# Kernel tuning notes

Hardware: AMD Instinct MI355X
Metric: run time of the kernel (lower is better)

Reference implementation:

```python
import jax, jax.numpy as jnp
import numpy as np

GX = GY = GZ = 128
VOXEL_DIM = 28  # 1 density + 27 SH coefficients (9 per RGB channel)
NUM_RAYS = 8192
NUM_SAMPLES = 128


def sh_basis(theta, phi):
    """Degree-2 SH basis in the coefficient order used by harmonic():
    [Y_0_0, Y_m1_1, Y_0_1, Y_1_1, Y_m2_2, Y_m1_2, Y_0_2, Y_1_2, Y_2_2]."""
    y00 = 0.5 * jnp.sqrt(1.0 / jnp.pi)
    h3 = 0.5 * jnp.sqrt(3.0 / jnp.pi)
    q5 = 0.25 * jnp.sqrt(5.0 / jnp.pi)
    h15 = 0.5 * jnp.sqrt(15.0 / jnp.pi)
    q15 = 0.25 * jnp.sqrt(15.0 / jnp.pi)
    st, ct = jnp.sin(theta), jnp.cos(theta)
    sp, cp = jnp.sin(phi), jnp.cos(phi)
    return jnp.stack([
        y00 * jnp.ones_like(theta),          # Y_0_0
        h3 * st * sp,                        # Y_m1_1
        h3 * ct,                             # Y_0_1
        h3 * st * cp,                        # Y_1_1
        h15 * st * cp * st * sp,             # Y_m2_2
        h15 * st * sp * ct,                  # Y_m1_2
        q5 * (3.0 * ct * ct - 1.0),          # Y_0_2
        h15 * st * cp * ct,                  # Y_1_2
        q15 * ((st * cp) ** 2 - (st * sp) ** 2),  # Y_2_2
    ])


def trilinear(grid, pos):
    """grid: [GX,GY,GZ,D]; pos: [R,S,3] -> [R,S,D] interpolated features."""
    p0 = jnp.floor(pos).astype(jnp.int32)
    fr = pos - p0.astype(pos.dtype)
    x0, y0, z0 = p0[..., 0], p0[..., 1], p0[..., 2]
    xd, yd, zd = fr[..., 0:1], fr[..., 1:2], fr[..., 2:3]
    c000 = grid[x0, y0, z0]
    c001 = grid[x0, y0, z0 + 1]
    c010 = grid[x0, y0 + 1, z0]
    c011 = grid[x0, y0 + 1, z0 + 1]
    c100 = grid[x0 + 1, y0, z0]
    c101 = grid[x0 + 1, y0, z0 + 1]
    c110 = grid[x0 + 1, y0 + 1, z0]
    c111 = grid[x0 + 1, y0 + 1, z0 + 1]
    c00 = c000 * (1 - xd) + c100 * xd
    c01 = c001 * (1 - xd) + c101 * xd
    c10 = c010 * (1 - xd) + c110 * xd
    c11 = c011 * (1 - xd) + c111 * xd
    c0 = c00 * (1 - yd) + c10 * yd
    c1 = c01 * (1 - yd) + c11 * yd
    return c0 * (1 - zd) + c1 * zd


def setup_inputs() -> dict:
    key = jax.random.key(0)
    k1, k2, k3, k4 = jax.random.split(key, 4)
    voxel_grid = jax.random.uniform(k1, (GX, GY, GZ, VOXEL_DIM), dtype=jnp.float32)
    # sample positions inside [0, G-2] so the +1 corner stays in bounds
    sample_positions = jax.random.uniform(
        k2, (NUM_RAYS, NUM_SAMPLES, 3), dtype=jnp.float32) * (GX - 2)
    sample_distances = jax.random.uniform(
        k3, (NUM_RAYS, NUM_SAMPLES), dtype=jnp.float32) * 0.1
    viewing_angle = jax.random.uniform(k4, (2,), dtype=jnp.float32) * np.pi
    return {
        "voxel_grid": voxel_grid,
        "sample_positions": sample_positions,
        "sample_distances": sample_distances,
        "viewing_angle": viewing_angle,
    }


def reference(voxel_grid, sample_positions, sample_distances, viewing_angle):
    R, S = sample_distances.shape
    feats = trilinear(voxel_grid, sample_positions)          # [R,S,28]
    sigma = feats[..., 0]                                     # [R,S]
    sh_coeffs = feats[..., 1:].reshape(R, S, 3, 9)            # [R,S,3,9]
    basis = sh_basis(viewing_angle[0], viewing_angle[1])      # [9]
    rgb = jnp.einsum('rsck,k->rsc', sh_coeffs, basis)         # [R,S,3]
    tau = sigma * sample_distances                            # [R,S]
    att = jnp.exp(-tau)
    # faithful to channel_opacity_z: transmittance is the CUMULATIVE SUM of
    # exp(-sigma_j * d_j) over j = 0..k (inclusive of current sample)
    transmittance = jnp.cumsum(att, axis=1)
    alpha = 1.0 - att
    weights = transmittance * alpha                           # [R,S]
    return jnp.sum(weights[..., None] * rgb, axis=1)          # [R,3]
```

## Files before the change

kernel.cpp:

```cpp
#include <hip/hip_runtime.h>
#include <hip/hip_fp16.h>
#include <math.h>

#define GXD 128
#define GYD 128
#define GZD 128
#define VD 28
#define VDP 32
#define NRAYS 8192
#define NSAMP 128

__global__ __launch_bounds__(256) void convert_grid(
    const float* __restrict__ g, __half* __restrict__ h)
{
    const unsigned t = blockIdx.x * 256u + threadIdx.x;
    const unsigned o = t << 1;
    const unsigned v = o >> 5;
    const unsigned k = o & 31;
    __half2 out;
    if (k < VD) {
        const float2 f = *(const float2*)(g + v * VD + k);
        out = __floats2half2_rn(f.x, f.y);
    } else {
        out = __floats2half2_rn(0.0f, 0.0f);
    }
    *(__half2*)(h + o) = out;
}

__global__ __launch_bounds__(1024) void plenoxel_fused16(
    const __half* __restrict__ hg,
    const float* __restrict__ pos,
    const float* __restrict__ dist,
    const float* __restrict__ ang,
    float* __restrict__ out)
{
    __shared__ float4 srgb[NSAMP];

    const int ray  = blockIdx.x;
    const int tid  = threadIdx.x;
    const int s    = tid >> 3;
    const int subl = tid & 7;
    const int dx   = (subl >> 2) & 1;
    const int dy   = (subl >> 1) & 1;
    const int zh   = subl & 1;

    const float theta = ang[0], phi = ang[1];
    float st, ct, sp, cp;
    sincosf(theta, &st, &ct);
    sincosf(phi,   &sp, &cp);
    float basis[9];
    basis[0] = 0.28209479177387814f;
    basis[1] = 0.4886025119029199f * st * sp;
    basis[2] = 0.4886025119029199f * ct;
    basis[3] = 0.4886025119029199f * st * cp;
    basis[4] = 1.0925484305920792f * st * cp * st * sp;
    basis[5] = 1.0925484305920792f * st * sp * ct;
    basis[6] = 0.31539156525252005f * (3.0f * ct * ct - 1.0f);
    basis[7] = 1.0925484305920792f * st * cp * ct;
    basis[8] = 0.5462742152960396f * ((st * cp) * (st * cp) - (st * sp) * (st * sp));

    const int sidx = ray * NSAMP + s;
    const float px = pos[sidx * 3 + 0];
    const float py = pos[sidx * 3 + 1];
    const float pz = pos[sidx * 3 + 2];
    const int ix = (int)floorf(px);
    const int iy = (int)floorf(py);
    const int iz = (int)floorf(pz);
    const float fx = px - (float)ix;
    const float fy = py - (float)iy;
    const float fz = pz - (float)iz;

    const float w = (dx ? fx : 1.0f - fx) *
                    (dy ? fy : 1.0f - fy) *
                    (zh ? fz : 1.0f - fz);

    const int base = (((ix + dx) * GYD + (iy + dy)) * GZD + (iz + zh)) * VDP;
    const float4* __restrict__ q = (const float4*)(hg + base);

    float4 raw[4];
    raw[0] = q[0]; raw[1] = q[1]; raw[2] = q[2]; raw[3] = q[3];
    const __half* f = (const __half*)raw;

    float sig = __half2float(f[0]);
    float r = 0.0f, g = 0.0f, b = 0.0f;
    #pragma unroll
    for (int k = 0; k < 9; ++k) {
        r += basis[k] * __half2float(f[1 + k]);
        g += basis[k] * __half2float(f[10 + k]);
        b += basis[k] * __half2float(f[19 + k]);
    }
    float psig = w * sig;
    float pr = w * r, pg = w * g, pb = w * b;

    #pragma unroll
    for (int off = 1; off < 8; off <<= 1) {
        psig += __shfl_xor(psig, off, 64);
        pr   += __shfl_xor(pr,   off, 64);
        pg   += __shfl_xor(pg,   off, 64);
        pb   += __shfl_xor(pb,   off, 64);
    }
    if (subl == 0) srgb[s] = make_float4(psig, pr, pg, pb);
    __syncthreads();

    if (tid < 64) {
        const int lane = tid;
        const float4 a0 = srgb[lane];
        const float4 a1 = srgb[lane + 64];
        const float d0 = dist[ray * NSAMP + lane];
        const float d1 = dist[ray * NSAMP + lane + 64];
        const float att0 = expf(-a0.x * d0);
        const float att1 = expf(-a1.x * d1);

        float scan_lo = att0;
        #pragma unroll
        for (int off = 1; off < 64; off <<= 1) {
            const float v = __shfl_up(scan_lo, off, 64);
            if (lane >= off) scan_lo += v;
        }
        const float total_lo = __shfl(scan_lo, 63, 64);

        float scan_hi = att1;
        #pragma unroll
        for (int off = 1; off < 64; off <<= 1) {
            const float v = __shfl_up(scan_hi, off, 64);
            if (lane >= off) scan_hi += v;
        }
        const float w_lo = scan_lo * (1.0f - att0);
        const float w_hi = (total_lo + scan_hi) * (1.0f - att1);

        float o0 = w_lo * a0.y + w_hi * a1.y;
        float o1 = w_lo * a0.z + w_hi * a1.z;
        float o2 = w_lo * a0.w + w_hi * a1.w;

        #pragma unroll
        for (int off = 32; off > 0; off >>= 1) {
            o0 += __shfl_xor(o0, off, 64);
            o1 += __shfl_xor(o1, off, 64);
            o2 += __shfl_xor(o2, off, 64);
        }
        if (lane == 0) {
            out[ray * 3 + 0] = o0;
            out[ray * 3 + 1] = o1;
            out[ray * 3 + 2] = o2;
        }
    }
}

__global__ __launch_bounds__(1024) void plenoxel_fused32(
    const float* __restrict__ grid,
    const float* __restrict__ pos,
    const float* __restrict__ dist,
    const float* __restrict__ ang,
    float* __restrict__ out)
{
    __shared__ float4 srgb[NSAMP];
    const int ray  = blockIdx.x;
    const int tid  = threadIdx.x;
    const int s    = tid >> 3;
    const int subl = tid & 7;
    const int dx   = (subl >> 2) & 1;
    const int dy   = (subl >> 1) & 1;
    const int zh   = subl & 1;

    const float theta = ang[0], phi = ang[1];
    float st, ct, sp, cp;
    sincosf(theta, &st, &ct);
    sincosf(phi,   &sp, &cp);
    float basis[9];
    basis[0] = 0.28209479177387814f;
    basis[1] = 0.4886025119029199f * st * sp;
    basis[2] = 0.4886025119029199f * ct;
    basis[3] = 0.4886025119029199f * st * cp;
    basis[4] = 1.0925484305920792f * st * cp * st * sp;
    basis[5] = 1.0925484305920792f * st * sp * ct;
    basis[6] = 0.31539156525252005f * (3.0f * ct * ct - 1.0f);
    basis[7] = 1.0925484305920792f * st * cp * ct;
    basis[8] = 0.5462742152960396f * ((st * cp) * (st * cp) - (st * sp) * (st * sp));

    const int sidx = ray * NSAMP + s;
    const float px = pos[sidx * 3 + 0];
    const float py = pos[sidx * 3 + 1];
    const float pz = pos[sidx * 3 + 2];
    const int ix = (int)floorf(px);
    const int iy = (int)floorf(py);
    const int iz = (int)floorf(pz);
    const float fx = px - (float)ix;
    const float fy = py - (float)iy;
    const float fz = pz - (float)iz;

    const float w = (dx ? fx : 1.0f - fx) *
                    (dy ? fy : 1.0f - fy) *
                    (zh ? fz : 1.0f - fz);

    const int base = (((ix + dx) * GYD + (iy + dy)) * GZD + (iz + zh)) * VD;
    const float4* __restrict__ q = (const float4*)(grid + base);
    float f[28];
    #pragma unroll
    for (int i = 0; i < 7; ++i)
        ((float4*)f)[i] = q[i];

    float psig = w * f[0];
    float pr = 0.0f, pg = 0.0f, pb = 0.0f;
    #pragma unroll
    for (int k = 0; k < 9; ++k) {
        pr += basis[k] * f[1 + k];
        pg += basis[k] * f[10 + k];
        pb += basis[k] * f[19 + k];
    }
    pr *= w; pg *= w; pb *= w;

    #pragma unroll
    for (int off = 1; off < 8; off <<= 1) {
        psig += __shfl_xor(psig, off, 64);
        pr   += __shfl_xor(pr,   off, 64);
        pg   += __shfl_xor(pg,   off, 64);
        pb   += __shfl_xor(pb,   off, 64);
    }
    if (subl == 0) srgb[s] = make_float4(psig, pr, pg, pb);
    __syncthreads();

    if (tid < 64) {
        const int lane = tid;
        const float4 a0 = srgb[lane];
        const float4 a1 = srgb[lane + 64];
        const float d0 = dist[ray * NSAMP + lane];
        const float d1 = dist[ray * NSAMP + lane + 64];
        const float att0 = expf(-a0.x * d0);
        const float att1 = expf(-a1.x * d1);

        float scan_lo = att0;
        #pragma unroll
        for (int off = 1; off < 64; off <<= 1) {
            const float v = __shfl_up(scan_lo, off, 64);
            if (lane >= off) scan_lo += v;
        }
        const float total_lo = __shfl(scan_lo, 63, 64);
        float scan_hi = att1;
        #pragma unroll
        for (int off = 1; off < 64; off <<= 1) {
            const float v = __shfl_up(scan_hi, off, 64);
            if (lane >= off) scan_hi += v;
        }
        const float w_lo = scan_lo * (1.0f - att0);
        const float w_hi = (total_lo + scan_hi) * (1.0f - att1);

        float o0 = w_lo * a0.y + w_hi * a1.y;
        float o1 = w_lo * a0.z + w_hi * a1.z;
        float o2 = w_lo * a0.w + w_hi * a1.w;
        #pragma unroll
        for (int off = 32; off > 0; off >>= 1) {
            o0 += __shfl_xor(o0, off, 64);
            o1 += __shfl_xor(o1, off, 64);
            o2 += __shfl_xor(o2, off, 64);
        }
        if (lane == 0) {
            out[ray * 3 + 0] = o0;
            out[ray * 3 + 1] = o1;
            out[ray * 3 + 2] = o2;
        }
    }
}

extern "C" void kernel_launch(void* const* d_in, const int* in_sizes, int n_in,
                              void* d_out, int out_size, void* d_ws, size_t ws_size,
                              hipStream_t stream) {
    const float* grid = (const float*)d_in[0];
    const float* pos  = (const float*)d_in[1];
    const float* dist = (const float*)d_in[2];
    const float* ang  = (const float*)d_in[3];
    float* out = (float*)d_out;

    const size_t need = (size_t)GXD * GYD * GZD * VDP * sizeof(__half);
    if (ws_size >= need) {
        __half* hg = (__half*)d_ws;
        const unsigned n_half2 = (unsigned)((size_t)GXD * GYD * GZD * VDP / 2);
        convert_grid<<<n_half2 / 256, 256, 0, stream>>>(grid, hg);
        plenoxel_fused16<<<NRAYS, 1024, 0, stream>>>(hg, pos, dist, ang, out);
    } else {
        plenoxel_fused32<<<NRAYS, 1024, 0, stream>>>(grid, pos, dist, ang, out);
    }
}
```

Measured before the change: 446.6 us.

## Pre-contract SH basis into per-voxel float4 grid before trilinear rendering

Because the SH dot product is linear and the viewing angle is shared by every sample, each voxel's 27 coefficients are reduced to RGB ahead of time, giving a packed (sigma,r,g,b) float4 grid. The render kernel then fetches eight float4 corners per sample in one thread, so the eight-lane split and its shuffle reduction go away, and it handles two rays per 256-thread block. The gather footprint per sample falls from 64 bytes of fp16 to 16 bytes of fp32, and fp16 rounding is gone. The preprocessing pass still has to read the whole fp32 grid every call.

```diff
diff --git a/kernel.cpp b/kernel.cpp
--- a/kernel.cpp
+++ b/kernel.cpp
@@ -1,65 +1,73 @@
 #include <hip/hip_runtime.h>
-#include <hip/hip_fp16.h>
 #include <math.h>
 
 #define GXD 128
 #define GYD 128
 #define GZD 128
 #define VD 28
-#define VDP 32
 #define NRAYS 8192
 #define NSAMP 128
-
-__global__ __launch_bounds__(256) void convert_grid(
-    const float* __restrict__ g, __half* __restrict__ h)
+#define NVOX (GXD * GYD * GZD)
+
+__global__ __launch_bounds__(256) void predot_grid(
+    const float* __restrict__ g,
+    const float* __restrict__ ang,
+    float4* __restrict__ o)
 {
-    const unsigned t = blockIdx.x * 256u + threadIdx.x;
-    const unsigned o = t << 1;
-    const unsigned v = o >> 5;
-    const unsigned k = o & 31;
-    __half2 out;
-    if (k < VD) {
-        const float2 f = *(const float2*)(g + v * VD + k);
-        out = __floats2half2_rn(f.x, f.y);
-    } else {
-        out = __floats2half2_rn(0.0f, 0.0f);
-    }
-    *(__half2*)(h + o) = out;
-}
-
-__global__ __launch_bounds__(1024) void plenoxel_fused16(
-    const __half* __restrict__ hg,
+    __shared__ float sb[9];
+    if (threadIdx.x == 0) {
+        float st, ct, sp, cp;
+        sincosf(ang[0], &st, &ct);
+        sincosf(ang[1], &sp, &cp);
+        sb[0] = 0.28209479177387814f;
+        sb[1] = 0.4886025119029199f * st * sp;
+        sb[2] = 0.4886025119029199f * ct;
+        sb[3] = 0.4886025119029199f * st * cp;
+        sb[4] = 1.0925484305920792f * st * cp * st * sp;
+        sb[5] = 1.0925484305920792f * st * sp * ct;
+        sb[6] = 0.31539156525252005f * (3.0f * ct * ct - 1.0f);
+        sb[7] = 1.0925484305920792f * st * cp * ct;
+        sb[8] = 0.5462742152960396f * ((st * cp) * (st * cp) - (st * sp) * (st * sp));
+    }
+    __syncthreads();
+
+    const int v = blockIdx.x * 256 + threadIdx.x;
+    const float4* __restrict__ p = (const float4*)(g + (size_t)v * VD);
+    float f[28];
+    #pragma unroll
+    for (int i = 0; i < 7; ++i)
+        ((float4*)f)[i] = p[i];
+
+    float r = 0.0f, gg = 0.0f, b = 0.0f;
+    #pragma unroll
+    for (int k = 0; k < 9; ++k) {
+        r  += sb[k] * f[1 + k];
+        gg += sb[k] * f[10 + k];
+        b  += sb[k] * f[19 + k];
+    }
+    o[v] = make_float4(f[0], r, gg, b);
+}
+
+#define LERP4(a, b, t) make_float4( \
+    fmaf((t), (b).x - (a).x, (a).x), \
+    fmaf((t), (b).y - (a).y, (a).y), \
+    fmaf((t), (b).z - (a).z, (a).z), \
+    fmaf((t), (b).w - (a).w, (a).w))
+
+__global__ __launch_bounds__(256) void render(
+    const float4* __restrict__ vg,
     const float* __restrict__ pos,
     const float* __restrict__ dist,
-    const float* __restrict__ ang,
     float* __restrict__ out)
 {
-    __shared__ float4 srgb[NSAMP];
-
-    const int ray  = blockIdx.x;
+    __shared__ float4 srgb[2][NSAMP];
+
     const int tid  = threadIdx.x;
-    const int s    = tid >> 3;
-    const int subl = tid & 7;
-    const int dx   = (subl >> 2) & 1;
-    const int dy   = (subl >> 1) & 1;
-    const int zh   = subl & 1;
-
-    const float theta = ang[0], phi = ang[1];
-    float st, ct, sp, cp;
-    sincosf(theta, &st, &ct);
-    sincosf(phi,   &sp, &cp);
-    float basis[9];
-    basis[0] = 0.28209479177387814f;
-    basis[1] = 0.4886025119029199f * st * sp;
-    basis[2] = 0.4886025119029199f * ct;
-    basis[3] = 0.4886025119029199f * st * cp;
-    basis[4] = 1.0925484305920792f * st * cp * st * sp;
-    basis[5] = 1.0925484305920792f * st * sp * ct;
-    basis[6] = 0.31539156525252005f * (3.0f * ct * ct - 1.0f);
-    basis[7] = 1.0925484305920792f * st * cp * ct;
-    basis[8] = 0.5462742152960396f * ((st * cp) * (st * cp) - (st * sp) * (st * sp));
-
+    const int rloc = tid >> 7;
+    const int s    = tid & 127;
+    const int ray  = blockIdx.x * 2 + rloc;
     const int sidx = ray * NSAMP + s;
+
     const float px = pos[sidx * 3 + 0];
     const float py = pos[sidx * 3 + 1];
     const float pz = pos[sidx * 3 + 2];
@@ -70,46 +78,35 @@
     const float fy = py - (float)iy;
     const float fz = pz - (float)iz;
 
-    const float w = (dx ? fx : 1.0f - fx) *
-                    (dy ? fy : 1.0f - fy) *
-                    (zh ? fz : 1.0f - fz);
-
-    const int base = (((ix + dx) * GYD + (iy + dy)) * GZD + (iz + zh)) * VDP;
-    const float4* __restrict__ q = (const float4*)(hg + base);
-
-    float4 raw[4];
-    raw[0] = q[0]; raw[1] = q[1]; raw[2] = q[2]; raw[3] = q[3];
-    const __half* f = (const __half*)raw;
-
-    float sig = __half2float(f[0]);
-    float r = 0.0f, g = 0.0f, b = 0.0f;
-    #pragma unroll
-    for (int k = 0; k < 9; ++k) {
-        r += basis[k] * __half2float(f[1 + k]);
-        g += basis[k] * __half2float(f[10 + k]);
-        b += basis[k] * __half2float(f[19 + k]);
-    }
-    float psig = w * sig;
-    float pr = w * r, pg = w * g, pb = w * b;
-
-    #pragma unroll
-    for (int off = 1; off < 8; off <<= 1) {
-        psig += __shfl_xor(psig, off, 64);
-        pr   += __shfl_xor(pr,   off, 64);
-        pg   += __shfl_xor(pg,   off, 64);
-        pb   += __shfl_xor(pb,   off, 64);
-    }
-    if (subl == 0) srgb[s] = make_float4(psig, pr, pg, pb);
+    const float4* __restrict__ c = vg + (((size_t)ix * GYD + iy) * GZD + iz);
+    const float4 c000 = c[0];
+    const float4 c001 = c[1];
+    const float4 c010 = c[GZD];
+    const float4 c011 = c[GZD + 1];
+    const float4 c100 = c[(size_t)GYD * GZD];
+    const float4 c101 = c[(size_t)GYD * GZD + 1];
+    const float4 c110 = c[(size_t)GYD * GZD + GZD];
+    const float4 c111 = c[(size_t)GYD * GZD + GZD + 1];
+
+    const float4 a00 = LERP4(c000, c001, fz);
+    const float4 a01 = LERP4(c010, c011, fz);
+    const float4 a10 = LERP4(c100, c101, fz);
+    const float4 a11 = LERP4(c110, c111, fz);
+    const float4 a0  = LERP4(a00, a01, fy);
+    const float4 a1  = LERP4(a10, a11, fy);
+    const float4 a   = LERP4(a0, a1, fx);
+
+    const float d   = dist[sidx];
+    const float att = expf(-a.x * d);
+    srgb[rloc][s] = make_float4(att, a.y, a.z, a.w);
     __syncthreads();
 
-    if (tid < 64) {
-        const int lane = tid;
-        const float4 a0 = srgb[lane];
-        const float4 a1 = srgb[lane + 64];
-        const float d0 = dist[ray * NSAMP + lane];
-        const float d1 = dist[ray * NSAMP + lane + 64];
-        const float att0 = expf(-a0.x * d0);
-        const float att1 = expf(-a1.x * d1);
+    if ((tid & 127) < 64) {
+        const int lane = tid & 63;
+        const float4 a0v = srgb[rloc][lane];
+        const float4 a1v = srgb[rloc][lane + 64];
+        const float att0 = a0v.x;
+        const float att1 = a1v.x;
 
         float scan_lo = att0;
         #pragma unroll
@@ -128,9 +125,9 @@
         const float w_lo = scan_lo * (1.0f - att0);
         const float w_hi = (total_lo + scan_hi) * (1.0f - att1);
 
-        float o0 = w_lo * a0.y + w_hi * a1.y;
-        float o1 = w_lo * a0.z + w_hi * a1.z;
-        float o2 = w_lo * a0.w + w_hi * a1.w;
+        float o0 = w_lo * a0v.y + w_hi * a1v.y;
+        float o1 = w_lo * a0v.z + w_hi * a1v.z;
+        float o2 = w_lo * a0v.w + w_hi * a1v.w;
 
         #pragma unroll
         for (int off = 32; off > 0; off >>= 1) {
@@ -270,12 +267,11 @@
     const float* ang  = (const float*)d_in[3];
     float* out = (float*)d_out;
 
-    const size_t need = (size_t)GXD * GYD * GZD * VDP * sizeof(__half);
+    const size_t need = (size_t)NVOX * sizeof(float4);
     if (ws_size >= need) {
-        __half* hg = (__half*)d_ws;
-        const unsigned n_half2 = (unsigned)((size_t)GXD * GYD * GZD * VDP / 2);
-        convert_grid<<<n_half2 / 256, 256, 0, stream>>>(grid, hg);
-        plenoxel_fused16<<<NRAYS, 1024, 0, stream>>>(hg, pos, dist, ang, out);
+        float4* vg = (float4*)d_ws;
+        predot_grid<<<NVOX / 256, 256, 0, stream>>>(grid, ang, vg);
+        render<<<NRAYS / 2, 256, 0, stream>>>(vg, pos, dist, out);
     } else {
         plenoxel_fused32<<<NRAYS, 1024, 0, stream>>>(grid, pos, dist, ang, out);
     }
```

Measured after the change: 399.8 us. 1.12x faster.
